# Performance work log

Measured on AMD Instinct MI355X. Metric: run time of the kernel, lower is better.

The kernel has to match this reference:

```python
import jax, jax.numpy as jnp
import numpy as np

B, S, D = 16, 1024, 768          # batch, seq_len, in_features
NS, MAXW = 256, 8                # num_spans, max span width (fixed for jit)
V, C = 128, 6                    # num_vertexes, max corefs per vertex
R = 512                          # num_max_rels_per_example
REL, HID, DIS = 97, 384, 20      # relation_num, hidden_dim, dis_size
NEG = -1e30


def setup_inputs() -> dict:
    key = jax.random.key(0)
    ks = jax.random.split(key, 14)
    sentence_repr = jax.random.normal(ks[0], (B, S, D), jnp.float32)
    starts = jax.random.randint(ks[1], (B, NS), 0, S - MAXW)
    widths = jax.random.randint(ks[2], (B, NS), 0, MAXW)
    entity_span_indices = jnp.stack([starts, starts + widths], axis=-1)  # (B,NS,2), start<=end
    entity_span_indices_mask = jax.random.randint(ks[3], (B, NS), 0, 2)
    vertex_indices = jax.random.randint(ks[4], (B, V, C), 0, NS)
    vertex_indices_mask = jax.random.randint(ks[5], (B, V, C), 0, 2)
    head_tail_indices = jax.random.randint(ks[6], (B, R, 2), 0, V)
    relation_mask = jax.random.randint(ks[7], (B, R), 0, 2)
    dis_h_2_t = jax.random.randint(ks[8], (B, R), 0, 20)
    dis_t_2_h = jax.random.randint(ks[9], (B, R), 0, 20)
    dis_embed = jax.random.normal(ks[10], (20, DIS), jnp.float32) * 0.02
    dis_embed = dis_embed.at[10].set(0.0)  # padding_idx=10
    fin = D + DIS                      # final_in_features with distance
    in_proj = 2 * fin + D              # concat [head+dis, tail+dis, head*tail]
    W1 = jax.random.normal(ks[11], (in_proj, HID), jnp.float32) / np.float32(np.sqrt(in_proj))
    W2 = jax.random.normal(ks[12], (HID, REL), jnp.float32) / np.float32(np.sqrt(HID))
    b2 = jnp.zeros((REL,), jnp.float32)
    return dict(sentence_repr=sentence_repr, entity_span_indices=entity_span_indices,
                entity_span_indices_mask=entity_span_indices_mask,
                vertex_indices=vertex_indices, vertex_indices_mask=vertex_indices_mask,
                head_tail_indices=head_tail_indices, relation_mask=relation_mask,
                dis_h_2_t=dis_h_2_t, dis_t_2_h=dis_t_2_h,
                dis_embed=dis_embed, W1=W1, W2=W2, b2=b2)


def reference(sentence_repr, entity_span_indices, entity_span_indices_mask,
              vertex_indices, vertex_indices_mask, head_tail_indices,
              relation_mask, dis_h_2_t, dis_t_2_h, dis_embed, W1, W2, b2):
    Bx, Sx, Dx = sentence_repr.shape
    # --- SpanExtractor: masked max pooling over tokens in each span [start, end] ---
    starts = entity_span_indices[..., 0]
    ends = entity_span_indices[..., 1]
    pos = starts[..., None] + jnp.arange(MAXW)            # (B,NS,W)
    valid = pos <= ends[..., None]
    posc = jnp.clip(pos, 0, Sx - 1).reshape(Bx, -1)       # (B,NS*W)
    tok = jnp.take_along_axis(sentence_repr, posc[..., None], axis=1)
    tok = tok.reshape(Bx, NS, MAXW, Dx)
    span_emb = jnp.where(valid[..., None], tok, NEG).max(axis=2)   # (B,NS,D)
    # --- coref 'mean' pooling over spans per vertex (batched_index_select) ---
    vidx = vertex_indices.reshape(Bx, -1)
    ve = jnp.take_along_axis(span_emb, vidx[..., None], axis=1).reshape(Bx, V, C, Dx)
    m = vertex_indices_mask.astype(jnp.float32)
    cnt = jnp.maximum(m.sum(axis=2), 1.0)                 # num_corefs clamped >=1
    vertex_emb = (ve * m[..., None]).sum(axis=2) / cnt[..., None]  # (B,V,D)
    # --- head/tail gather ---
    hti = head_tail_indices.reshape(Bx, -1)
    ht = jnp.take_along_axis(vertex_emb, hti[..., None], axis=1).reshape(Bx, R, 2, Dx)
    head_repr = ht[:, :, 0, :]
    tail_repr = ht[:, :, 1, :]
    # (original multiplies by relation_mask and discards the result -> no-op)
    eh = dis_embed[dis_h_2_t]                              # (B,R,DIS)
    et = dis_embed[dis_t_2_h]
    feat = jnp.concatenate([head_repr, eh, tail_repr, et, head_repr * tail_repr], axis=-1)
    # TwoLayerLinear: relu(x @ W1) @ W2 + b2, bias=(False, True)
    predict_re = jax.nn.relu(feat @ W1) @ W2 + b2          # (B,R,REL)
    return predict_re
```

## Files before the change

### kernel.cpp

```cpp
#include <hip/hip_runtime.h>
#include <cstdint>
#include <cstddef>

#define B_    16
#define S_    1024
#define D_    768
#define NS_   256
#define V_    128
#define C_    6
#define R_    512
#define REL_  97
#define HID_  384
#define DIS_  20
#define K1_   2344
#define KP_   2432
#define NIT_  38
#define N2P_  128

#define BM1   128
#define BN1   128
#define SLICE_ ((size_t)8192 * HID_)

typedef unsigned short ushort_t;
typedef unsigned int   u32;
typedef short bf16x4 __attribute__((ext_vector_type(4)));
typedef short bf16x8 __attribute__((ext_vector_type(8)));
typedef float f32x4  __attribute__((ext_vector_type(4)));
typedef float f32x16 __attribute__((ext_vector_type(16)));

__device__ __forceinline__ float bf2f(short s) {
    return __uint_as_float(((unsigned int)(unsigned short)s) << 16);
}
__device__ __forceinline__ short f2bf(float x) {
    union { float f; unsigned int u; } c; c.f = x;
    unsigned int r = (c.u + 0x7fffu + ((c.u >> 16) & 1u)) >> 16;
    return (short)(unsigned short)r;
}

typedef const __attribute__((address_space(1))) u32* gas_t;
typedef __attribute__((address_space(3))) u32*       las_t;
__device__ __forceinline__ void dma16(const void* g, void* l) {
    __builtin_amdgcn_global_load_lds((gas_t)g, (las_t)l, 16, 0, 0);
}

__device__ __forceinline__ int w1_orig(int k) {
    if      (k < 768)  return k;
    else if (k < 1536) return k + 20;
    else if (k < 2304) return k + 40;
    else if (k < 2324) return 768 + (k - 2304);
    else if (k < K1_)  return 1556 + (k - 2324);
    return -1;
}

__global__ __launch_bounds__(256) void prep_kernel(
    const float* __restrict__ sr, const int* __restrict__ spans,
    const float* __restrict__ W1, const float* __restrict__ W2,
    ushort_t* __restrict__ span_emb, ushort_t* __restrict__ W1Tile,
    ushort_t* __restrict__ W2T)
{
    int blk = blockIdx.x;
    int tid = threadIdx.x;
    if (blk < 4096) {
        int bn    = blk;
        int b     = bn >> 8;
        int start = spans[2 * bn];
        int end   = spans[2 * bn + 1];
        int w     = end - start;
        const float* base = sr + ((size_t)b * S_ + start) * D_;
        ushort_t* out = span_emb + (size_t)bn * D_;
#pragma unroll
        for (int e = 0; e < 3; ++e) {
            int d = tid + e * 256;
            float x[8];
#pragma unroll
            for (int j = 0; j < 8; ++j)
                x[j] = base[(size_t)j * D_ + d];
            float m = x[0];
#pragma unroll
            for (int j = 1; j < 8; ++j)
                m = (j <= w) ? fmaxf(m, x[j]) : m;
            out[d] = (ushort_t)f2bf(m);
        }
    } else if (blk < 4096 + 456) {
        int flat = (blk - 4096) * 256 + tid;
        int nn   = flat & 127;
        int kg   = (flat >> 7) & 7;
        int itnt = flat >> 10;
        int nt   = itnt % 3;
        int it   = itnt / 3;
        int n    = nt * 128 + nn;
        bf16x8 p;
#pragma unroll
        for (int j = 0; j < 8; ++j) {
            int k = it * 64 + kg * 8 + j;
            int orig = w1_orig(k);
            float v = (orig >= 0) ? W1[(size_t)orig * HID_ + n] : 0.f;
            p[j] = f2bf(v);
        }
        *(bf16x8*)(W1Tile + (((size_t)itnt * 8 + kg) * 1024) + nn * 8) = p;
    } else {
        int g  = (blk - 4552) * 256 + tid;
        int n  = g / 48;
        int k0 = (g - n * 48) * 8;
        bf16x8 p;
#pragma unroll
        for (int j = 0; j < 8; ++j) {
            float v = (n < REL_) ? W2[(size_t)(k0 + j) * REL_ + n] : 0.f;
            p[j] = f2bf(v);
        }
        *(bf16x8*)(W2T + (size_t)n * HID_ + k0) = p;
    }
}

__global__ __launch_bounds__(192) void vertex_kernel(
    const ushort_t* __restrict__ span_emb, const int* __restrict__ vidx,
    const int* __restrict__ vmask, ushort_t* __restrict__ vembB)
{
    int bv = blockIdx.x;
    int b  = bv >> 7;
    const int* vi = vidx  + bv * C_;
    const int* vm = vmask + bv * C_;
    int   idxs[C_];
    float ms[C_];
    float cnt = 0.f;
#pragma unroll
    for (int c = 0; c < C_; ++c) {
        idxs[c] = vi[c];
        ms[c]   = (float)vm[c];
        cnt    += ms[c];
    }
    float inv = 1.f / fmaxf(cnt, 1.f);
    int col = threadIdx.x * 4;
    float s[4] = {0.f, 0.f, 0.f, 0.f};
#pragma unroll
    for (int c = 0; c < C_; ++c) {
        if (ms[c] != 0.f) {
            bf16x4 x = *(const bf16x4*)(span_emb +
                        ((size_t)(b * NS_ + idxs[c])) * D_ + col);
#pragma unroll
            for (int q = 0; q < 4; ++q) s[q] += bf2f(x[q]);
        }
    }
    bf16x4 o;
#pragma unroll
    for (int q = 0; q < 4; ++q) o[q] = f2bf(s[q] * inv);
    *(bf16x4*)(vembB + (size_t)bv * D_ + col) = o;
}

__global__ __launch_bounds__(256, 2) void gemm1_kernel(
    const ushort_t* __restrict__ vembB, const int* __restrict__ ht,
    const int* __restrict__ dht, const int* __restrict__ dth,
    const float* __restrict__ dis, const ushort_t* __restrict__ W1Tile,
    ushort_t* __restrict__ hiddenS)
{
    __shared__ ushort_t Abuf[2][BM1][64];
    __shared__ ushort_t Bbuf[2][8][BN1][8];

    int tid  = threadIdx.x;
    int wv   = tid >> 6;
    int lane = tid & 63;
    int m0   = blockIdx.x * BM1;
    int n0   = blockIdx.y * BN1;
    int nt   = blockIdx.y;
    int ksl  = blockIdx.z;

    int rr  = lane >> 3;
    int sl  = lane & 7;
    int gsw = (sl - rr) & 7;

    int hoff[4], toff[4];
#pragma unroll
    for (int gi = 0; gi < 4; ++gi) {
        int row = wv * 32 + gi * 8 + rr;
        int g   = m0 + row;
        int b   = g >> 9;
        hoff[gi] = (b * V_ + ht[2 * g])     * D_;
        toff[gi] = (b * V_ + ht[2 * g + 1]) * D_;
    }

    auto stage = [&](int bf, int it_g) {
        int k0   = it_g * 64;
        int r    = k0 / 768;
        int koff = k0 - r * 768;
        int kk   = koff + gsw * 8;
        if (r == 0) {
#pragma unroll
            for (int gi = 0; gi < 4; ++gi)
                dma16(vembB + hoff[gi] + kk, &Abuf[bf][wv * 32 + gi * 8][0]);
        } else if (r == 1) {
#pragma unroll
            for (int gi = 0; gi < 4; ++gi)
                dma16(vembB + toff[gi] + kk, &Abuf[bf][wv * 32 + gi * 8][0]);
        } else if (r == 2) {
#pragma unroll
            for (int gi = 0; gi < 4; ++gi) {
                bf16x8 h = *(const bf16x8*)(vembB + hoff[gi] + kk);
                bf16x8 t = *(const bf16x8*)(vembB + toff[gi] + kk);
                bf16x8 p;
#pragma unroll
                for (int j = 0; j < 8; ++j) p[j] = f2bf(bf2f(h[j]) * bf2f(t[j]));
                *(bf16x8*)&Abuf[bf][wv * 32 + gi * 8 + rr][sl * 8] = p;
            }
        } else {
            int kb = k0 - 2304;
#pragma unroll
            for (int gi = 0; gi < 4; ++gi) {
                int g   = m0 + wv * 32 + gi * 8 + rr;
                int rdh = dht[g], rdt = dth[g];
                bf16x8 p;
#pragma unroll
                for (int j = 0; j < 8; ++j) {
                    int kkj = kb + gsw * 8 + j;
                    float v = 0.f;
                    if      (kkj < 20) v = dis[rdh * DIS_ + kkj];
                    else if (kkj < 40) v = dis[rdt * DIS_ + (kkj - 20)];
                    p[j] = f2bf(v);
                }
                *(bf16x8*)&Abuf[bf][wv * 32 + gi * 8 + rr][sl * 8] = p;
            }
        }
        const ushort_t* bbase = W1Tile + ((size_t)it_g * 3 + nt) * 8192;
#pragma unroll
        for (int q = 0; q < 4; ++q) {
            int p = wv * 4 + q;
            dma16(bbase + (size_t)p * 512 + lane * 8,
                  &Bbuf[bf][p >> 1][(p & 1) * 64][0]);
        }
    };

    int half = lane >> 5;
    int lrow = lane & 31;
    int wm   = (wv & 1) * 64;
    int wn   = (wv >> 1) * 64;

    f32x16 acc[2][2];
#pragma unroll
    for (int i = 0; i < 2; ++i)
#pragma unroll
        for (int j = 0; j < 2; ++j)
#pragma unroll
            for (int r = 0; r < 16; ++r) acc[i][j][r] = 0.f;

    stage(0, ksl);
    for (int it = 0; it < 19; ++it) {
        int bf = it & 1;
        __syncthreads();
        if (it + 1 < 19) stage(bf ^ 1, 2 * (it + 1) + ksl);
#pragma unroll
        for (int s = 0; s < 4; ++s) {
            int kg   = s * 2 + half;
            int slot = ((kg + lrow) & 7) * 8;
            bf16x8 a0 = *(bf16x8*)&Abuf[bf][wm + lrow][slot];
            bf16x8 a1 = *(bf16x8*)&Abuf[bf][wm + 32 + lrow][slot];
            bf16x8 b0 = *(bf16x8*)&Bbuf[bf][kg][wn + lrow][0];
            bf16x8 b1 = *(bf16x8*)&Bbuf[bf][kg][wn + 32 + lrow][0];
            acc[0][0] = __builtin_amdgcn_mfma_f32_32x32x16_bf16(a0, b0, acc[0][0], 0, 0, 0);
            acc[0][1] = __builtin_amdgcn_mfma_f32_32x32x16_bf16(a0, b1, acc[0][1], 0, 0, 0);
            acc[1][0] = __builtin_amdgcn_mfma_f32_32x32x16_bf16(a1, b0, acc[1][0], 0, 0, 0);
            acc[1][1] = __builtin_amdgcn_mfma_f32_32x32x16_bf16(a1, b1, acc[1][1], 0, 0, 0);
        }
    }

    ushort_t* outp = hiddenS + (size_t)ksl * SLICE_;
#pragma unroll
    for (int fm = 0; fm < 2; ++fm)
#pragma unroll
        for (int fn = 0; fn < 2; ++fn) {
            int col = n0 + wn + fn * 32 + lrow;
#pragma unroll
            for (int r = 0; r < 16; ++r) {
                int row = m0 + wm + fm * 32 + (r & 3) + 8 * (r >> 2) + 4 * half;
                outp[(size_t)row * HID_ + col] = (ushort_t)f2bf(acc[fm][fn][r]);
            }
        }
}

__global__ __launch_bounds__(256) void gemm2_kernel(
    const ushort_t* __restrict__ hiddenS, const ushort_t* __restrict__ W2T,
    const float* __restrict__ b2, float* __restrict__ out)
{
    __shared__ ushort_t As[32][72];
    __shared__ ushort_t Bs[128][72];

    int m0  = blockIdx.x * 32;
    int tid = threadIdx.x;

    int arow = tid >> 3;
    int akk  = (tid & 7) * 8;

    bf16x8 pA; bf16x8 pB[4];
    auto loadAB = [&](int k0) {
        const ushort_t* hp = hiddenS + (size_t)(m0 + arow) * HID_ + k0 + akk;
        bf16x8 x0 = *(const bf16x8*)hp;
        bf16x8 x1 = *(const bf16x8*)(hp + SLICE_);
#pragma unroll
        for (int j = 0; j < 8; ++j)
            pA[j] = f2bf(fmaxf(bf2f(x0[j]) + bf2f(x1[j]), 0.f));
#pragma unroll
        for (int e = 0; e < 4; ++e)
            pB[e] = *(const bf16x8*)(W2T + (size_t)(arow + e * 32) * HID_ + k0 + akk);
    };

    int w    = tid >> 6;
    int lane = tid & 63;
    int wm = (w & 1) * 16;
    int wn = (w >> 1) * 64;
    int lr = lane & 15, lq = lane >> 4;

    f32x4 acc[4];
#pragma unroll
    for (int e = 0; e < 4; ++e) acc[e] = (f32x4){0.f, 0.f, 0.f, 0.f};

    loadAB(0);
    for (int k0 = 0; k0 < HID_; k0 += 64) {
        __syncthreads();
        *(bf16x8*)&As[arow][akk] = pA;
#pragma unroll
        for (int e = 0; e < 4; ++e)
            *(bf16x8*)&Bs[arow + e * 32][akk] = pB[e];
        __syncthreads();
        if (k0 + 64 < HID_) loadAB(k0 + 64);
#pragma unroll
        for (int ks = 0; ks < 2; ++ks) {
            int kb = ks * 32 + lq * 8;
            bf16x8 a = *(bf16x8*)&As[wm + lr][kb];
#pragma unroll
            for (int nf = 0; nf < 4; ++nf) {
                bf16x8 bb = *(bf16x8*)&Bs[wn + nf * 16 + lr][kb];
                acc[nf] = __builtin_amdgcn_mfma_f32_16x16x32_bf16(a, bb, acc[nf], 0, 0, 0);
            }
        }
    }

    int grow = m0 + wm + lq * 4;
#pragma unroll
    for (int nf = 0; nf < 4; ++nf) {
        int col = wn + nf * 16 + lr;
        if (col < REL_) {
            float bias = b2[col];
#pragma unroll
            for (int r = 0; r < 4; ++r)
                out[(size_t)(grow + r) * REL_ + col] = acc[nf][r] + bias;
        }
    }
}

extern "C" void kernel_launch(void* const* d_in, const int* in_sizes, int n_in,
                              void* d_out, int out_size, void* d_ws, size_t ws_size,
                              hipStream_t stream)
{
    const float* sr    = (const float*)d_in[0];
    const int*   spans = (const int*)  d_in[1];
    const int*   vidx  = (const int*)  d_in[3];
    const int*   vmask = (const int*)  d_in[4];
    const int*   ht    = (const int*)  d_in[5];
    const int*   dht   = (const int*)  d_in[7];
    const int*   dth   = (const int*)  d_in[8];
    const float* dis   = (const float*)d_in[9];
    const float* W1    = (const float*)d_in[10];
    const float* W2    = (const float*)d_in[11];
    const float* b2    = (const float*)d_in[12];
    float* out = (float*)d_out;

    ushort_t* span_emb = (ushort_t*)d_ws;
    ushort_t* vembB    = span_emb + (size_t)B_ * NS_ * D_;
    ushort_t* W1Tile   = vembB + (size_t)B_ * V_ * D_;
    ushort_t* W2T      = W1Tile + (size_t)NIT_ * 3 * 8192;
    ushort_t* hiddenS  = W2T + (size_t)N2P_ * HID_;

    prep_kernel<<<4096 + 456 + 24, 256, 0, stream>>>(
        sr, spans, W1, W2, span_emb, W1Tile, W2T);
    vertex_kernel<<<B_ * V_, 192, 0, stream>>>(span_emb, vidx, vmask, vembB);

    dim3 g1((B_ * R_) / BM1, HID_ / BN1, 2);
    gemm1_kernel<<<g1, 256, 0, stream>>>(vembB, ht, dht, dth, dis, W1Tile, hiddenS);

    gemm2_kernel<<<(B_ * R_) / 32, 256, 0, stream>>>(hiddenS, W2T, b2, out);
}
```

Before: 154.2 us.

## Halve GEMM1 N-tile to 64 and vectorize span max-pool with 192 threads

GEMM1's N tile drops from 128 to 64, which doubles the grid to 64x6x2 blocks. Each wave now computes a 64x32 sub-tile with two MFMA accumulators, and the launch bound allows three blocks per SM. The W1 pre-tiling layout in prep_kernel is rewritten to match the 64-wide tiles. The span max-pool now uses 192 threads, each loading float4 vectors. The intent is better occupancy and load balance across CUs for the small GEMM, at the cost of reloading the A tile twice as often and doing less MFMA work per LDS read.

```diff
diff --git a/kernel.cpp b/kernel.cpp
--- a/kernel.cpp
+++ b/kernel.cpp
@@ -18,7 +18,7 @@
 #define N2P_  128
 
 #define BM1   128
-#define BN1   128
+#define BN1   64
 #define SLICE_ ((size_t)8192 * HID_)
 
 typedef unsigned short ushort_t;
@@ -52,7 +52,7 @@
     return -1;
 }
 
-__global__ __launch_bounds__(256) void prep_kernel(
+__global__ __launch_bounds__(192) void prep_kernel(
     const float* __restrict__ sr, const int* __restrict__ spans,
     const float* __restrict__ W1, const float* __restrict__ W2,
     ushort_t* __restrict__ span_emb, ushort_t* __restrict__ W1Tile,
@@ -66,40 +66,40 @@
         int start = spans[2 * bn];
         int end   = spans[2 * bn + 1];
         int w     = end - start;
-        const float* base = sr + ((size_t)b * S_ + start) * D_;
-        ushort_t* out = span_emb + (size_t)bn * D_;
-#pragma unroll
-        for (int e = 0; e < 3; ++e) {
-            int d = tid + e * 256;
-            float x[8];
-#pragma unroll
-            for (int j = 0; j < 8; ++j)
-                x[j] = base[(size_t)j * D_ + d];
-            float m = x[0];
-#pragma unroll
-            for (int j = 1; j < 8; ++j)
-                m = (j <= w) ? fmaxf(m, x[j]) : m;
-            out[d] = (ushort_t)f2bf(m);
-        }
-    } else if (blk < 4096 + 456) {
-        int flat = (blk - 4096) * 256 + tid;
-        int nn   = flat & 127;
-        int kg   = (flat >> 7) & 7;
-        int itnt = flat >> 10;
-        int nt   = itnt % 3;
-        int it   = itnt / 3;
-        int n    = nt * 128 + nn;
+        const float* base = sr + ((size_t)b * S_ + start) * D_ + tid * 4;
+        f32x4 x[8];
+#pragma unroll
+        for (int j = 0; j < 8; ++j)
+            x[j] = *(const f32x4*)(base + (size_t)j * D_);
+        f32x4 m = x[0];
+#pragma unroll
+        for (int j = 1; j < 8; ++j)
+            if (j <= w) {
+#pragma unroll
+                for (int c = 0; c < 4; ++c) m[c] = fmaxf(m[c], x[j][c]);
+            }
+        bf16x4 o;
+#pragma unroll
+        for (int c = 0; c < 4; ++c) o[c] = f2bf(m[c]);
+        *(bf16x4*)(span_emb + (size_t)bn * D_ + tid * 4) = o;
+    } else if (blk < 4096 + 608) {
+        int flat = (blk - 4096) * 192 + tid;
+        int nn   = flat & 63;
+        int kg   = (flat >> 6) & 7;
+        int itnt = flat >> 9;
+        int it   = itnt / 6;
         bf16x8 p;
 #pragma unroll
         for (int j = 0; j < 8; ++j) {
             int k = it * 64 + kg * 8 + j;
             int orig = w1_orig(k);
+            int n    = (itnt - it * 6) * 64 + nn;
             float v = (orig >= 0) ? W1[(size_t)orig * HID_ + n] : 0.f;
             p[j] = f2bf(v);
         }
-        *(bf16x8*)(W1Tile + (((size_t)itnt * 8 + kg) * 1024) + nn * 8) = p;
+        *(bf16x8*)(W1Tile + ((size_t)itnt * 8 + kg) * 512 + nn * 8) = p;
     } else {
-        int g  = (blk - 4552) * 256 + tid;
+        int g  = (blk - 4704) * 192 + tid;
         int n  = g / 48;
         int k0 = (g - n * 48) * 8;
         bf16x8 p;
@@ -147,7 +147,7 @@
     *(bf16x4*)(vembB + (size_t)bv * D_ + col) = o;
 }
 
-__global__ __launch_bounds__(256, 2) void gemm1_kernel(
+__global__ __launch_bounds__(256, 3) void gemm1_kernel(
     const ushort_t* __restrict__ vembB, const int* __restrict__ ht,
     const int* __restrict__ dht, const int* __restrict__ dth,
     const float* __restrict__ dis, const ushort_t* __restrict__ W1Tile,
@@ -219,27 +219,24 @@
                 *(bf16x8*)&Abuf[bf][wv * 32 + gi * 8 + rr][sl * 8] = p;
             }
         }
-        const ushort_t* bbase = W1Tile + ((size_t)it_g * 3 + nt) * 8192;
-#pragma unroll
-        for (int q = 0; q < 4; ++q) {
-            int p = wv * 4 + q;
-            dma16(bbase + (size_t)p * 512 + lane * 8,
-                  &Bbuf[bf][p >> 1][(p & 1) * 64][0]);
+        const ushort_t* bbase = W1Tile + ((size_t)it_g * 6 + nt) * 4096;
+#pragma unroll
+        for (int q = 0; q < 2; ++q) {
+            int p = wv * 2 + q;
+            dma16(bbase + (size_t)p * 512 + lane * 8, &Bbuf[bf][p][0][0]);
         }
     };
 
     int half = lane >> 5;
     int lrow = lane & 31;
     int wm   = (wv & 1) * 64;
-    int wn   = (wv >> 1) * 64;
-
-    f32x16 acc[2][2];
+    int wn   = (wv >> 1) * 32;
+
+    f32x16 acc[2];
 #pragma unroll
     for (int i = 0; i < 2; ++i)
 #pragma unroll
-        for (int j = 0; j < 2; ++j)
-#pragma unroll
-            for (int r = 0; r < 16; ++r) acc[i][j][r] = 0.f;
+        for (int r = 0; r < 16; ++r) acc[i][r] = 0.f;
 
     stage(0, ksl);
     for (int it = 0; it < 19; ++it) {
@@ -253,26 +250,21 @@
             bf16x8 a0 = *(bf16x8*)&Abuf[bf][wm + lrow][slot];
             bf16x8 a1 = *(bf16x8*)&Abuf[bf][wm + 32 + lrow][slot];
             bf16x8 b0 = *(bf16x8*)&Bbuf[bf][kg][wn + lrow][0];
-            bf16x8 b1 = *(bf16x8*)&Bbuf[bf][kg][wn + 32 + lrow][0];
-            acc[0][0] = __builtin_amdgcn_mfma_f32_32x32x16_bf16(a0, b0, acc[0][0], 0, 0, 0);
-            acc[0][1] = __builtin_amdgcn_mfma_f32_32x32x16_bf16(a0, b1, acc[0][1], 0, 0, 0);
-            acc[1][0] = __builtin_amdgcn_mfma_f32_32x32x16_bf16(a1, b0, acc[1][0], 0, 0, 0);
-            acc[1][1] = __builtin_amdgcn_mfma_f32_32x32x16_bf16(a1, b1, acc[1][1], 0, 0, 0);
+            acc[0] = __builtin_amdgcn_mfma_f32_32x32x16_bf16(a0, b0, acc[0], 0, 0, 0);
+            acc[1] = __builtin_amdgcn_mfma_f32_32x32x16_bf16(a1, b0, acc[1], 0, 0, 0);
         }
     }
 
     ushort_t* outp = hiddenS + (size_t)ksl * SLICE_;
-#pragma unroll
-    for (int fm = 0; fm < 2; ++fm)
-#pragma unroll
-        for (int fn = 0; fn < 2; ++fn) {
-            int col = n0 + wn + fn * 32 + lrow;
-#pragma unroll
-            for (int r = 0; r < 16; ++r) {
-                int row = m0 + wm + fm * 32 + (r & 3) + 8 * (r >> 2) + 4 * half;
-                outp[(size_t)row * HID_ + col] = (ushort_t)f2bf(acc[fm][fn][r]);
-            }
-        }
+    int col = n0 + wn + lrow;
+#pragma unroll
+    for (int fm = 0; fm < 2; ++fm) {
+#pragma unroll
+        for (int r = 0; r < 16; ++r) {
+            int row = m0 + wm + fm * 32 + (r & 3) + 8 * (r >> 2) + 4 * half;
+            outp[(size_t)row * HID_ + col] = (ushort_t)f2bf(acc[fm][r]);
+        }
+    }
 }
 
 __global__ __launch_bounds__(256) void gemm2_kernel(
@@ -365,10 +357,10 @@
     ushort_t* span_emb = (ushort_t*)d_ws;
     ushort_t* vembB    = span_emb + (size_t)B_ * NS_ * D_;
     ushort_t* W1Tile   = vembB + (size_t)B_ * V_ * D_;
-    ushort_t* W2T      = W1Tile + (size_t)NIT_ * 3 * 8192;
+    ushort_t* W2T      = W1Tile + (size_t)NIT_ * 6 * 4096;
     ushort_t* hiddenS  = W2T + (size_t)N2P_ * HID_;
 
-    prep_kernel<<<4096 + 456 + 24, 256, 0, stream>>>(
+    prep_kernel<<<4096 + 608 + 32, 192, 0, stream>>>(
         sr, spans, W1, W2, span_emb, W1Tile, W2T);
     vertex_kernel<<<B_ * V_, 192, 0, stream>>>(span_emb, vidx, vmask, vembB);
 
```

After: 154.6 us. No clear change (+0.2%).
